# Kernel optimization log

Measured on AMD Instinct MI355X. Metric: run time of the kernel, lower is better.

Reference implementation:

```python
import jax, jax.numpy as jnp
import numpy as np

DX = 8e-6      # pixel pitch (m)
Z = 0.05       # propagation distance (m)
B, C, H, W = 8, 3, 1024, 1024


def setup_inputs() -> dict:
    key = jax.random.key(0)
    k1, k2 = jax.random.split(key)
    x_real = jax.random.normal(k1, (B, C, H, W), dtype=jnp.float32)
    x_imag = jax.random.normal(k2, (B, C, H, W), dtype=jnp.float32)
    wavelengths = jnp.asarray([450e-9, 532e-9, 632.8e-9], dtype=jnp.float32)
    return {"x_real": x_real, "x_imag": x_imag, "wavelengths": wavelengths}


def _transfer_function(wavelengths, h, w, dx, z):
    # Angular-spectrum transfer function per wavelength: [C, H, W] complex64
    fx = jnp.fft.fftfreq(w, d=dx).astype(jnp.float32)  # [W]
    fy = jnp.fft.fftfreq(h, d=dx).astype(jnp.float32)  # [H]
    f2 = fy[:, None] ** 2 + fx[None, :] ** 2           # [H, W]
    lam = wavelengths[:, None, None]                   # [C, 1, 1]
    arg = 1.0 - (lam ** 2) * f2[None]                  # [C, H, W]
    kz = (2.0 * jnp.pi / lam) * z * jnp.sqrt(jnp.maximum(arg, 0.0))
    Hc = jnp.exp(1j * kz.astype(jnp.complex64))
    # zero out evanescent components
    return jnp.where(arg > 0.0, Hc, jnp.zeros((), dtype=jnp.complex64))


def reference(x_real, x_imag, wavelengths):
    # Batched angular-spectrum propagation, one wavelength per channel.
    x = (x_real + 1j * x_imag).astype(jnp.complex64)   # [B, C, H, W]
    Hc = _transfer_function(wavelengths, H, W, DX, Z)  # [C, H, W]
    Xf = jnp.fft.fft2(x, axes=(-2, -1))
    out = jnp.fft.ifft2(Xf * Hc[None], axes=(-2, -1))  # [B, C, H, W] complex
    # return real/imag stacked so output is a float tensor: [2, B, C, H, W]
    return jnp.stack([out.real.astype(jnp.float32), out.imag.astype(jnp.float32)], axis=0)
```

## Files before the change

kernel.cpp:

```cpp
#include <hip/hip_runtime.h>
#include <math.h>


#define NIMG 24

__device__ __forceinline__ float2 cadd(float2 a, float2 b){ return make_float2(a.x+b.x, a.y+b.y); }
__device__ __forceinline__ float2 csub(float2 a, float2 b){ return make_float2(a.x-b.x, a.y-b.y); }
__device__ __forceinline__ float2 cmul(float2 a, float c, float s){ return make_float2(a.x*c - a.y*s, a.x*s + a.y*c); }

__device__ __forceinline__ int SW(int j) {
    int b = j << 3;
    return b ^ (((b >> 7) & 7) << 4);
}

__device__ __forceinline__ float2 computeH(float lam, int ky, int kx) {
    int iy = (ky < 512) ? ky : ky - 1024;
    int ix = (kx < 512) ? kx : kx - 1024;
    const double recip = 1.0 / (1024.0 * 8e-06);
    float fy = (float)((double)iy * recip);
    float fx = (float)((double)ix * recip);
    float f2  = __fadd_rn(__fmul_rn(fy, fy), __fmul_rn(fx, fx));
    float l2  = __fmul_rn(lam, lam);
    float arg = __fsub_rn(1.0f, __fmul_rn(l2, f2));
    float2 h = make_float2(0.0f, 0.0f);
    if (arg > 0.0f) {
        float t  = __fdiv_rn(6.28318530717958647692f, lam);
        t        = __fmul_rn(t, 0.05f);
        float kz = __fmul_rn(t, __fsqrt_rn(arg));
        double s, c;
        sincos((double)kz, &s, &c);
        const float sc = 9.5367431640625e-07f;
        h = make_float2((float)c * sc, (float)s * sc);
    }
    return h;
}

__global__ __launch_bounds__(256) void build_H_T(float2* __restrict__ Htab,
                                                 const float* __restrict__ wl) {
    int idx = blockIdx.x * 256 + threadIdx.x;
    int c   = idx >> 20;
    int rem = idx & 1048575;
    Htab[idx] = computeH(wl[c], rem & 1023, rem >> 10);
}

template<int SIGN>
__device__ __forceinline__ void dft4nt(float2& a0, float2& a1, float2& a2, float2& a3) {
    float2 t0 = cadd(a0, a2), t1 = csub(a0, a2);
    float2 t2 = cadd(a1, a3), t3 = csub(a1, a3);
    a0 = cadd(t0, t2);
    a2 = csub(t0, t2);
    a1 = make_float2(t1.x - SIGN * t3.y, t1.y + SIGN * t3.x);
    a3 = make_float2(t1.x + SIGN * t3.y, t1.y - SIGN * t3.x);
}
template<int SIGN>
__device__ __forceinline__ void dft4(float2& a0, float2& a1, float2& a2, float2& a3,
                                     float c1, float s1) {
    float c2 = c1*c1 - s1*s1, s2 = 2.f*c1*s1;
    float c3 = c2*c1 - s2*s1, s3 = s2*c1 + c2*s1;
    a1 = cmul(a1, c1, s1);
    a2 = cmul(a2, c2, s2);
    a3 = cmul(a3, c3, s3);
    dft4nt<SIGN>(a0, a1, a2, a3);
}

#define WSYNC() do { asm volatile("s_waitcnt lgkmcnt(0)" ::: "memory"); \
                     __builtin_amdgcn_wave_barrier(); } while (0)


__device__ __forceinline__ void ldsToRegs(char* cb, int l, float2 (&v)[4][4]) {
    const int swzE = (((l >> 4)    ) & 7) << 4;
    const int swzO = (((l >> 4) + 4) & 7) << 4;
    char* rbE = cb + ((8 * l) ^ swzE);
    char* rbO = cb + ((8 * l) ^ swzO);
    #pragma unroll
    for (int k = 0; k < 4; ++k) {
        #pragma unroll
        for (int r = 0; r < 4; ++r) {
            const int tt = k + 4 * r;
            v[k][r] = *(const float2*)(((tt & 1) ? rbO : rbE) + 512 * tt);
        }
    }
}
__device__ __forceinline__ void regsToLds(char* cb, int l, const float2 (&v)[4][4]) {
    const int swzE = (((l >> 4)    ) & 7) << 4;
    const int swzO = (((l >> 4) + 4) & 7) << 4;
    char* rbE = cb + ((8 * l) ^ swzE);
    char* rbO = cb + ((8 * l) ^ swzO);
    #pragma unroll
    for (int m = 0; m < 4; ++m) {
        #pragma unroll
        for (int q = 0; q < 4; ++q) {
            const int tt = m + 4 * q;
            *(float2*)(((tt & 1) ? rbO : rbE) + 512 * tt) = v[m][q];
        }
    }
}

template<int SIGN>
__device__ __forceinline__ void fftA(char* cb, int l, float2 (&v)[4][4]) {
    const float SPI8 = SIGN * 0.39269908169872415481f;
    #pragma unroll
    for (int k = 0; k < 4; ++k) dft4nt<SIGN>(v[k][0], v[k][1], v[k][2], v[k][3]);
    dft4nt<SIGN>(v[0][0], v[1][0], v[2][0], v[3][0]);
    #pragma unroll
    for (int q = 1; q < 4; ++q) {
        float s1, c1; __sincosf((float)q * SPI8, &s1, &c1);
        dft4<SIGN>(v[0][q], v[1][q], v[2][q], v[3][q], c1, s1);
    }
    char* wb = cb + 128 * l;
    const int L7 = l & 7;
    #pragma unroll
    for (int p = 0; p < 4; ++p) {
        *(float4*)(wb + 16 * ((2*p+0) ^ L7)) =
            make_float4(v[p][0].x, v[p][0].y, v[p][1].x, v[p][1].y);
        *(float4*)(wb + 16 * ((2*p+1) ^ L7)) =
            make_float4(v[p][2].x, v[p][2].y, v[p][3].x, v[p][3].y);
    }
}

template<int SIGN>
__device__ __forceinline__ void fftB(char* cb, int l) {
    const float SPI32  = SIGN * 0.09817477042468103870f;
    const float SPI128 = SIGN * 0.02454369260617025967f;
    const int swzE = (((l >> 4)    ) & 7) << 4;
    const int swzO = (((l >> 4) + 4) & 7) << 4;
    char* rbE = cb + ((8 * l) ^ swzE);
    char* rbO = cb + ((8 * l) ^ swzO);
    float2 v[4][4];
    #pragma unroll
    for (int k = 0; k < 4; ++k) {
        #pragma unroll
        for (int r = 0; r < 4; ++r) {
            const int tt = k + 4 * r;
            v[k][r] = *(const float2*)(((tt & 1) ? rbO : rbE) + 512 * tt);
        }
    }
    const int jm2 = l & 15;
    float s1, c1; __sincosf((float)jm2 * SPI32, &s1, &c1);
    #pragma unroll
    for (int k = 0; k < 4; ++k) dft4<SIGN>(v[k][0], v[k][1], v[k][2], v[k][3], c1, s1);
    const int lo8 = 8 * (l & 15);
    const int hi  = 2048 * (l >> 4);
    #pragma unroll
    for (int q = 0; q < 4; ++q) {
        float s1b, c1b; __sincosf((float)(jm2 + 16 * q) * SPI128, &s1b, &c1b);
        dft4<SIGN>(v[0][q], v[1][q], v[2][q], v[3][q], c1b, s1b);
        #pragma unroll
        for (int p = 0; p < 4; ++p) {
            const int K = ((q + 4 * p) & 7) << 4;
            *(float2*)(cb + (lo8 ^ K) + hi + 128 * q + 512 * p) = v[p][q];
        }
    }
}

template<int SIGN>
__device__ __forceinline__ void fftC(int l, float2 (&v)[4][4]) {
    const float SPI512 = SIGN * 0.00613592315154256492f;
    #pragma unroll
    for (int m = 0; m < 4; ++m) {
        float s1, c1; __sincosf((float)(l + 64 * m) * SPI512, &s1, &c1);
        dft4<SIGN>(v[m][0], v[m][1], v[m][2], v[m][3], c1, s1);
    }
}

__global__ __launch_bounds__(1024) void k1_rows_T16(const float* __restrict__ xr,
                                                    const float* __restrict__ xi,
                                                    float2* __restrict__ T) {
    extern __shared__ char lds[];
    const int t = threadIdx.x, w = t >> 6, l = t & 63;
    const int img = blockIdx.x >> 6;
    const int y0  = (blockIdx.x & 63) << 4;
    const long long ib = (long long)img << 20;
    char* cb = lds + 8192 * w;

    const float* rr = xr + ib + (long long)(y0 + w) * 1024;
    const float* ri = xi + ib + (long long)(y0 + w) * 1024;
    float2 v[4][4];
    #pragma unroll
    for (int k = 0; k < 4; ++k) {
        #pragma unroll
        for (int r = 0; r < 4; ++r) {
            const int p = l + 64 * (k + 4 * r);
            v[k][r] = make_float2(rr[p], ri[p]);
        }
    }
    fftA<-1>(cb, l, v); WSYNC();
    fftB<-1>(cb, l);    WSYNC();
    ldsToRegs(cb, l, v);
    fftC<-1>(l, v);
    WSYNC();
    regsToLds(cb, l, v);
    __syncthreads();

    {
        float4* dst = (float4*)(T + ib + (long long)t * 1024 + y0);
        const int sx = SW(t);
        #pragma unroll
        for (int p = 0; p < 8; ++p) {
            float2 a = *(const float2*)(lds + 8192 * (2 * p)     + sx);
            float2 b = *(const float2*)(lds + 8192 * (2 * p + 1) + sx);
            dst[p] = make_float4(a.x, a.y, b.x, b.y);
        }
    }
}

__global__ __launch_bounds__(256, 4) void k2_cols_H(float2* __restrict__ T,
                                                    const float2* __restrict__ Htab,
                                                    const float* __restrict__ wl) {
    __shared__ float4 ldsb[2048];
    char* lds = (char*)ldsb;
    const int t = threadIdx.x, w = t >> 6, l = t & 63;
    const int img = blockIdx.x >> 8;
    const int x   = ((blockIdx.x & 255) << 2) + w;
    const int lamIdx = img % 3;
    char* cb = lds + 8192 * w;
    float2* col = T + ((long long)img << 20) + (long long)x * 1024;

    float2 v[4][4];
    #pragma unroll
    for (int k = 0; k < 4; ++k) {
        #pragma unroll
        for (int r = 0; r < 4; ++r)
            v[k][r] = col[l + 64 * (k + 4 * r)];
    }
    fftA<-1>(cb, l, v); WSYNC();
    fftB<-1>(cb, l);    WSYNC();

    float2 h[4][4];
    if (Htab) {
        const float2* hrow = Htab + ((long long)lamIdx << 20) + (long long)x * 1024;
        #pragma unroll
        for (int m = 0; m < 4; ++m) {
            #pragma unroll
            for (int q = 0; q < 4; ++q)
                h[m][q] = hrow[l + 64 * (m + 4 * q)];
        }
    } else {
        const float lam = wl[lamIdx];
        #pragma unroll
        for (int m = 0; m < 4; ++m) {
            #pragma unroll
            for (int q = 0; q < 4; ++q)
                h[m][q] = computeH(lam, l + 64 * (m + 4 * q), x);
        }
    }

    ldsToRegs(cb, l, v);
    fftC<-1>(l, v);

    #pragma unroll
    for (int m = 0; m < 4; ++m) {
        #pragma unroll
        for (int q = 0; q < 4; ++q) {
            float2 a = v[m][q], hh = h[m][q];
            v[m][q] = make_float2(a.x * hh.x - a.y * hh.y, a.x * hh.y + a.y * hh.x);
        }
    }
    WSYNC();

    fftA<1>(cb, l, v); WSYNC();
    fftB<1>(cb, l);    WSYNC();
    ldsToRegs(cb, l, v);
    fftC<1>(l, v);

    #pragma unroll
    for (int m = 0; m < 4; ++m) {
        #pragma unroll
        for (int q = 0; q < 4; ++q)
            col[l + 64 * (m + 4 * q)] = v[m][q];
    }
}

__global__ __launch_bounds__(1024) void k3_irows_T16(const float2* __restrict__ T,
                                                     float* __restrict__ outr,
                                                     float* __restrict__ outi) {
    extern __shared__ char lds[];
    const int t = threadIdx.x, w = t >> 6, l = t & 63;
    const int img = blockIdx.x >> 6;
    const int y0  = (blockIdx.x & 63) << 4;
    const long long ib = (long long)img << 20;

    {
        const float4* src = (const float4*)(T + ib + (long long)t * 1024 + y0);
        const int sx = SW(t);
        #pragma unroll
        for (int p = 0; p < 8; ++p) {
            float4 g = src[p];
            *(float2*)(lds + 8192 * (2 * p)     + sx) = make_float2(g.x, g.y);
            *(float2*)(lds + 8192 * (2 * p + 1) + sx) = make_float2(g.z, g.w);
        }
    }
    __syncthreads();

    char* cb = lds + 8192 * w;
    float2 v[4][4];
    ldsToRegs(cb, l, v);
    fftA<1>(cb, l, v); WSYNC();
    fftB<1>(cb, l);    WSYNC();
    ldsToRegs(cb, l, v);
    fftC<1>(l, v);

    float* pr = outr + ib + (long long)(y0 + w) * 1024;
    float* pi = outi + ib + (long long)(y0 + w) * 1024;
    #pragma unroll
    for (int m = 0; m < 4; ++m) {
        #pragma unroll
        for (int q = 0; q < 4; ++q) {
            const int p = l + 64 * (m + 4 * q);
            pr[p] = v[m][q].x;
            pi[p] = v[m][q].y;
        }
    }
}

extern "C" void kernel_launch(void* const* d_in, const int* in_sizes, int n_in,
                              void* d_out, int out_size, void* d_ws, size_t ws_size,
                              hipStream_t stream) {
    const float* xr = (const float*)d_in[0];
    const float* xi = (const float*)d_in[1];
    const float* wl = (const float*)d_in[2];
    float* out = (float*)d_out;

    const size_t planeElems = (size_t)NIMG * 1024 * 1024;
    float2* wsC = (float2*)d_ws;
    const size_t needC = planeElems * sizeof(float2);
    const size_t needH = (size_t)3 * 1024 * 1024 * sizeof(float2);
    float2* Htab = nullptr;
    if (ws_size >= needC + needH) {
        Htab = (float2*)((char*)d_ws + needC);
        build_H_T<<<12288, 256, 0, stream>>>(Htab, wl);
    }
    k1_rows_T16<<<NIMG * 64, 1024, 131072, stream>>>(xr, xi, wsC);
    k2_cols_H<<<NIMG * 256, 256, 0, stream>>>(wsC, Htab, wl);
    k3_irows_T16<<<NIMG * 64, 1024, 131072, stream>>>(wsC, out, out + planeElems);
}
```

Baseline: 322.6 us.

## Use 8-row chunked intermediate layout and process images in two halves

The intermediate spectrum moves from a transposed layout to an 8-row chunked layout: each 1024x1024 plane is stored as 128 groups of 8 rows, with each column's 8 values for a group contiguous. The row kernels now use 512-thread blocks over 8 rows with static LDS, and the column kernel reads strided through the chunks. The 24 images are processed in two batches of 12 so the workspace is half as large and may stay resident in the large last-level cache between kernels. The cost is six kernel launches instead of three, smaller row blocks, and more scattered 64-byte column accesses.

```diff
diff --git a/kernel.cpp b/kernel.cpp
--- a/kernel.cpp
+++ b/kernel.cpp
@@ -3,6 +3,7 @@
 
 
 #define NIMG 24
+#define HALF 12
 
 __device__ __forceinline__ float2 cadd(float2 a, float2 b){ return make_float2(a.x+b.x, a.y+b.y); }
 __device__ __forceinline__ float2 csub(float2 a, float2 b){ return make_float2(a.x-b.x, a.y-b.y); }
@@ -35,12 +36,15 @@
     return h;
 }
 
-__global__ __launch_bounds__(256) void build_H_T(float2* __restrict__ Htab,
-                                                 const float* __restrict__ wl) {
+__global__ __launch_bounds__(256) void build_H_C8(float2* __restrict__ Htab,
+                                                  const float* __restrict__ wl) {
     int idx = blockIdx.x * 256 + threadIdx.x;
     int c   = idx >> 20;
     int rem = idx & 1048575;
-    Htab[idx] = computeH(wl[c], rem & 1023, rem >> 10);
+    int yg8 = rem >> 13;
+    int kx  = (rem >> 3) & 1023;
+    int yi  = rem & 7;
+    Htab[idx] = computeH(wl[c], (yg8 << 3) | yi, kx);
 }
 
 template<int SIGN>
@@ -163,18 +167,21 @@
     }
 }
 
-__global__ __launch_bounds__(1024) void k1_rows_T16(const float* __restrict__ xr,
-                                                    const float* __restrict__ xi,
-                                                    float2* __restrict__ T) {
-    extern __shared__ char lds[];
+__global__ __launch_bounds__(512, 4) void k1_rows_C8(const float* __restrict__ xr,
+                                                     const float* __restrict__ xi,
+                                                     float2* __restrict__ T,
+                                                     int imgBase) {
+    __shared__ float4 ldsb[4096];
+    char* lds = (char*)ldsb;
     const int t = threadIdx.x, w = t >> 6, l = t & 63;
-    const int img = blockIdx.x >> 6;
-    const int y0  = (blockIdx.x & 63) << 4;
-    const long long ib = (long long)img << 20;
+    const int img_l = blockIdx.x >> 7;
+    const int yg8   = blockIdx.x & 127;
+    const int y0    = yg8 << 3;
     char* cb = lds + 8192 * w;
 
-    const float* rr = xr + ib + (long long)(y0 + w) * 1024;
-    const float* ri = xi + ib + (long long)(y0 + w) * 1024;
+    const long long gib = (long long)(imgBase + img_l) << 20;
+    const float* rr = xr + gib + (long long)(y0 + w) * 1024;
+    const float* ri = xi + gib + (long long)(y0 + w) * 1024;
     float2 v[4][4];
     #pragma unroll
     for (int k = 0; k < 4; ++k) {
@@ -193,47 +200,54 @@
     __syncthreads();
 
     {
-        float4* dst = (float4*)(T + ib + (long long)t * 1024 + y0);
-        const int sx = SW(t);
-        #pragma unroll
-        for (int p = 0; p < 8; ++p) {
-            float2 a = *(const float2*)(lds + 8192 * (2 * p)     + sx);
-            float2 b = *(const float2*)(lds + 8192 * (2 * p + 1) + sx);
-            dst[p] = make_float4(a.x, a.y, b.x, b.y);
-        }
-    }
-}
-
-__global__ __launch_bounds__(256, 4) void k2_cols_H(float2* __restrict__ T,
-                                                    const float2* __restrict__ Htab,
-                                                    const float* __restrict__ wl) {
+        const long long cb0 = ((long long)img_l << 20) + (long long)yg8 * 8192;
+        #pragma unroll
+        for (int c2 = 0; c2 < 2; ++c2) {
+            const int x = t + 512 * c2;
+            const int sx = SW(x);
+            float4* dst = (float4*)(T + cb0 + (long long)x * 8);
+            #pragma unroll
+            for (int p = 0; p < 4; ++p) {
+                float2 a = *(const float2*)(lds + 8192 * (2 * p)     + sx);
+                float2 b = *(const float2*)(lds + 8192 * (2 * p + 1) + sx);
+                dst[p] = make_float4(a.x, a.y, b.x, b.y);
+            }
+        }
+    }
+}
+
+__global__ __launch_bounds__(256, 4) void k2_cols_C8(float2* __restrict__ T,
+                                                     const float2* __restrict__ Htab,
+                                                     const float* __restrict__ wl) {
     __shared__ float4 ldsb[2048];
     char* lds = (char*)ldsb;
     const int t = threadIdx.x, w = t >> 6, l = t & 63;
-    const int img = blockIdx.x >> 8;
-    const int x   = ((blockIdx.x & 255) << 2) + w;
-    const int lamIdx = img % 3;
+    const int img_l = blockIdx.x >> 8;
+    const int x     = ((blockIdx.x & 255) << 2) + w;
+    const int lamIdx = img_l % 3;
     char* cb = lds + 8192 * w;
-    float2* col = T + ((long long)img << 20) + (long long)x * 1024;
+
+    const int laneOff = ((l >> 3) << 13) + x * 8 + (l & 7);
+    const int ib = (int)(img_l << 20);
 
     float2 v[4][4];
     #pragma unroll
     for (int k = 0; k < 4; ++k) {
         #pragma unroll
         for (int r = 0; r < 4; ++r)
-            v[k][r] = col[l + 64 * (k + 4 * r)];
+            v[k][r] = T[ib + laneOff + (k + 4 * r) * 65536];
     }
     fftA<-1>(cb, l, v); WSYNC();
     fftB<-1>(cb, l);    WSYNC();
 
     float2 h[4][4];
     if (Htab) {
-        const float2* hrow = Htab + ((long long)lamIdx << 20) + (long long)x * 1024;
+        const int hb = lamIdx << 20;
         #pragma unroll
         for (int m = 0; m < 4; ++m) {
             #pragma unroll
             for (int q = 0; q < 4; ++q)
-                h[m][q] = hrow[l + 64 * (m + 4 * q)];
+                h[m][q] = Htab[hb + laneOff + (m + 4 * q) * 65536];
         }
     } else {
         const float lam = wl[lamIdx];
@@ -267,27 +281,34 @@
     for (int m = 0; m < 4; ++m) {
         #pragma unroll
         for (int q = 0; q < 4; ++q)
-            col[l + 64 * (m + 4 * q)] = v[m][q];
-    }
-}
-
-__global__ __launch_bounds__(1024) void k3_irows_T16(const float2* __restrict__ T,
-                                                     float* __restrict__ outr,
-                                                     float* __restrict__ outi) {
-    extern __shared__ char lds[];
+            T[ib + laneOff + (m + 4 * q) * 65536] = v[m][q];
+    }
+}
+
+__global__ __launch_bounds__(512, 4) void k3_irows_C8(const float2* __restrict__ T,
+                                                      float* __restrict__ outr,
+                                                      float* __restrict__ outi,
+                                                      int imgBase) {
+    __shared__ float4 ldsb[4096];
+    char* lds = (char*)ldsb;
     const int t = threadIdx.x, w = t >> 6, l = t & 63;
-    const int img = blockIdx.x >> 6;
-    const int y0  = (blockIdx.x & 63) << 4;
-    const long long ib = (long long)img << 20;
+    const int img_l = blockIdx.x >> 7;
+    const int yg8   = blockIdx.x & 127;
+    const int y0    = yg8 << 3;
 
     {
-        const float4* src = (const float4*)(T + ib + (long long)t * 1024 + y0);
-        const int sx = SW(t);
-        #pragma unroll
-        for (int p = 0; p < 8; ++p) {
-            float4 g = src[p];
-            *(float2*)(lds + 8192 * (2 * p)     + sx) = make_float2(g.x, g.y);
-            *(float2*)(lds + 8192 * (2 * p + 1) + sx) = make_float2(g.z, g.w);
+        const long long cb0 = ((long long)img_l << 20) + (long long)yg8 * 8192;
+        #pragma unroll
+        for (int c2 = 0; c2 < 2; ++c2) {
+            const int x = t + 512 * c2;
+            const int sx = SW(x);
+            const float4* src = (const float4*)(T + cb0 + (long long)x * 8);
+            #pragma unroll
+            for (int p = 0; p < 4; ++p) {
+                float4 g = src[p];
+                *(float2*)(lds + 8192 * (2 * p)     + sx) = make_float2(g.x, g.y);
+                *(float2*)(lds + 8192 * (2 * p + 1) + sx) = make_float2(g.z, g.w);
+            }
         }
     }
     __syncthreads();
@@ -300,8 +321,9 @@
     ldsToRegs(cb, l, v);
     fftC<1>(l, v);
 
-    float* pr = outr + ib + (long long)(y0 + w) * 1024;
-    float* pi = outi + ib + (long long)(y0 + w) * 1024;
+    const long long gib = (long long)(imgBase + img_l) << 20;
+    float* pr = outr + gib + (long long)(y0 + w) * 1024;
+    float* pi = outi + gib + (long long)(y0 + w) * 1024;
     #pragma unroll
     for (int m = 0; m < 4; ++m) {
         #pragma unroll
@@ -322,15 +344,18 @@
     float* out = (float*)d_out;
 
     const size_t planeElems = (size_t)NIMG * 1024 * 1024;
-    float2* wsC = (float2*)d_ws;
-    const size_t needC = planeElems * sizeof(float2);
+    float2* T = (float2*)d_ws;
+    const size_t needT = (size_t)HALF * 1024 * 1024 * sizeof(float2);
     const size_t needH = (size_t)3 * 1024 * 1024 * sizeof(float2);
     float2* Htab = nullptr;
-    if (ws_size >= needC + needH) {
-        Htab = (float2*)((char*)d_ws + needC);
-        build_H_T<<<12288, 256, 0, stream>>>(Htab, wl);
-    }
-    k1_rows_T16<<<NIMG * 64, 1024, 131072, stream>>>(xr, xi, wsC);
-    k2_cols_H<<<NIMG * 256, 256, 0, stream>>>(wsC, Htab, wl);
-    k3_irows_T16<<<NIMG * 64, 1024, 131072, stream>>>(wsC, out, out + planeElems);
-}
+    if (ws_size >= needT + needH) {
+        Htab = (float2*)((char*)d_ws + needT);
+        build_H_C8<<<12288, 256, 0, stream>>>(Htab, wl);
+    }
+    for (int h = 0; h < 2; ++h) {
+        const int imgBase = h * HALF;
+        k1_rows_C8<<<HALF * 128, 512, 0, stream>>>(xr, xi, T, imgBase);
+        k2_cols_C8<<<HALF * 256, 256, 0, stream>>>(T, Htab, wl);
+        k3_irows_C8<<<HALF * 128, 512, 0, stream>>>(T, out, out + planeElems, imgBase);
+    }
+}
```

Result: slower. 336.1 us (+4.2%).
